# Kernel tuning notes

Measured on AMD Instinct MI355X. Metric: run time of the kernel, lower is better.

Reference implementation:

```python
import jax, jax.numpy as jnp
import numpy as np

N_ROW = 50000
N_COL = 50000
E = 600000
D = 128
NEG_SLOPE = 0.01  # torch LeakyReLU default


def _leaky(x):
    return jnp.where(x >= 0, x, NEG_SLOPE * x)


def _mlp(x, W1, b1, W2, b2):
    # (Linear -> LeakyReLU) x2, matching nn.Sequential in Conv_layer
    h = _leaky(x @ W1 + b1)
    return _leaky(h @ W2 + b2)


def setup_inputs() -> dict:
    key = jax.random.key(0)
    ks = jax.random.split(key, 16)
    inp = {
        "feat_row": jax.random.normal(ks[0], (N_ROW, D), jnp.float32),
        "feat_col": jax.random.normal(ks[1], (N_COL, D), jnp.float32),
        "src_c2r": jax.random.randint(ks[2], (E,), 0, N_COL, jnp.int32),
        "dst_c2r": jax.random.randint(ks[3], (E,), 0, N_ROW, jnp.int32),
        "w_c2r": jax.random.uniform(ks[4], (E,), jnp.float32),
        "src_r2c": jax.random.randint(ks[5], (E,), 0, N_ROW, jnp.int32),
        "dst_r2c": jax.random.randint(ks[6], (E,), 0, N_COL, jnp.int32),
        "w_r2c": jax.random.uniform(ks[7], (E,), jnp.float32),
        "W1_c2r": jax.random.normal(ks[8], (D, D), jnp.float32) / np.sqrt(D),
        "b1_c2r": jax.random.normal(ks[9], (D,), jnp.float32) * 0.01,
        "W2_c2r": jax.random.normal(ks[10], (D, D), jnp.float32) / np.sqrt(D),
        "b2_c2r": jax.random.normal(ks[11], (D,), jnp.float32) * 0.01,
        "W1_r2c": jax.random.normal(ks[12], (D, D), jnp.float32) / np.sqrt(D),
        "b1_r2c": jax.random.normal(ks[13], (D,), jnp.float32) * 0.01,
        "W2_r2c": jax.random.normal(ks[14], (D, D), jnp.float32) / np.sqrt(D),
        "b2_r2c": jax.random.normal(ks[15], (D,), jnp.float32) * 0.01,
        "eps_c2r": jnp.zeros((), jnp.float32),  # DGL GINConv init_eps=0
        "eps_r2c": jnp.zeros((), jnp.float32),
    }
    return inp


def reference(feat_row, feat_col, src_c2r, dst_c2r, w_c2r, src_r2c, dst_r2c, w_r2c,
              W1_c2r, b1_c2r, W2_c2r, b2_c2r, W1_r2c, b1_r2c, W2_r2c, b2_r2c,
              eps_c2r, eps_r2c):
    # col -> row GINConv (edge-weighted sum aggregation)
    msg = feat_col[src_c2r] * w_c2r[:, None]                       # [E, D]
    agg_row = jax.ops.segment_sum(msg, dst_c2r, num_segments=N_ROW)
    h_row = _mlp((1.0 + eps_c2r) * feat_row + agg_row, W1_c2r, b1_c2r, W2_c2r, b2_c2r)
    # row -> col GINConv using updated row features
    msg2 = h_row[src_r2c] * w_r2c[:, None]                         # [E, D]
    agg_col = jax.ops.segment_sum(msg2, dst_r2c, num_segments=N_COL)
    h_col = _mlp((1.0 + eps_r2c) * feat_col + agg_col, W1_r2c, b1_r2c, W2_r2c, b2_r2c)
    # residual (use_residual=True): add pre-conv embeddings
    return h_row + feat_row, h_col + feat_col
```

## Files before the change

kernel.cpp:

```cpp
#include <hip/hip_runtime.h>
#include <hip/hip_bf16.h>

#define NROW 50000
#define NCOL 50000
#define DDIM 128
#define CAP  32

typedef __bf16 bf16_t;
typedef __bf16 bf16x2 __attribute__((ext_vector_type(2)));
typedef __bf16 bf16x8 __attribute__((ext_vector_type(8)));
typedef float  f32x4  __attribute__((ext_vector_type(4)));

__device__ __forceinline__ float lrelu(float v) { return v >= 0.f ? v : 0.01f * v; }

__device__ __forceinline__ float ldf(const void* p, size_t i, bool f) {
    return f ? ((const float*)p)[i] : (float)((const bf16_t*)p)[i];
}

__device__ __forceinline__ bool dtf(const int* flags, int fi) {
    return (fi == -1) ? true : (fi == -2) ? false : (flags[fi] != 0);
}

struct TensorTab { const void* p[18]; int n[18]; };

__global__ __launch_bounds__(256) void detect_dtypes(TensorTab T, int* flags)
{
    __shared__ int vb, vf;
    const int tid = threadIdx.x;
    for (int t = 0; t < 18; ++t) {
        if (tid == 0) { vb = 0; vf = 0; }
        __syncthreads();
        const int n = T.n[t];
        const bool isFloatArr = (t != 2 && t != 3 && t != 5 && t != 6) && n >= 2;
        if (isFloatArr) {
            int nw = n / 2;
            int wi = (int)(((long long)tid * nw) >> 8);
            unsigned w = ((const unsigned*)T.p[t])[wi];
            unsigned low = w & 0xffffu;
            if (low) {
                int e = (int)((low >> 7) & 0xffu);
                if (e >= 90 && e <= 141) atomicAdd(&vb, 1);
                else                     atomicAdd(&vf, 1);
            }
        }
        __syncthreads();
        if (tid == 0) flags[t] = (isFloatArr && vf > vb) ? 1 : 0;
        __syncthreads();
    }
}

struct WPtrs { const void* W[4]; int fi[4]; };

__global__ __launch_bounds__(256) void prep_weights(WPtrs P, const int* flags,
                                                    __bf16* outp)
{
    int slot = blockIdx.x * 256 + threadIdx.x;
    if (slot >= 4 * 2048) return;
    int m = slot >> 11, sIdx = slot & 2047;
    bool f = flags[P.fi[m]] != 0;
    int l = sIdx & 63, combo = sIdx >> 6;
    int ct = combo >> 2, kk = combo & 3;
    int col  = ct * 16 + (l & 15);
    int krow = kk * 32 + (l >> 4) * 8;
    bf16x8 v;
#pragma unroll
    for (int j = 0; j < 8; ++j)
        v[j] = (__bf16)ldf(P.W[m], (size_t)(krow + j) * DDIM + col, f);
    ((bf16x8*)outp)[slot] = v;
}

__global__ __launch_bounds__(256) void convert_bf16(
    const void* __restrict__ in, __bf16* __restrict__ out, int n8,
    const int* __restrict__ flags, int fi)
{
    const bool f = dtf(flags, fi);
    int i = blockIdx.x * 256 + threadIdx.x;
    if (i >= n8) return;
    bf16x8 v;
    if (f) {
        f32x4 a = ((const f32x4*)in)[i * 2];
        f32x4 b = ((const f32x4*)in)[i * 2 + 1];
#pragma unroll
        for (int j = 0; j < 4; ++j) { v[j] = (__bf16)a[j]; v[j + 4] = (__bf16)b[j]; }
    } else {
        v = ((const bf16x8*)in)[i];
    }
    ((bf16x8*)out)[i] = v;
}

__global__ __launch_bounds__(256) void fill_slots_packed(
    const int* __restrict__ dst, const int* __restrict__ srcArr,
    const void* __restrict__ wArr, int nE, int* __restrict__ counts,
    int2* __restrict__ slots2, int* __restrict__ ovCount,
    int* __restrict__ ovList, const int* __restrict__ flags, int fiW)
{
    int e = blockIdx.x * 256 + threadIdx.x;
    if (e >= nE) return;
    const bool fW = dtf(flags, fiW);
    int d = dst[e];
    int pos = atomicAdd(&counts[d], 1);
    if (pos < CAP) {
        int2 pk;
        pk.x = srcArr[e];
        pk.y = __float_as_int(ldf(wArr, e, fW));
        slots2[(size_t)d * CAP + pos] = pk;
    } else {
        int k = atomicAdd(ovCount, 1);
        ovList[k] = e;
    }
}

__global__ __launch_bounds__(256) void scatter_overflow(
    const void* __restrict__ feat, const int* __restrict__ srcArr,
    const int* __restrict__ dstArr, const void* __restrict__ wArr,
    const int* __restrict__ ovList, const int* __restrict__ ovCount,
    float* __restrict__ agg, const int* __restrict__ flags, int fiFeat, int fiW)
{
    const bool fF = dtf(flags, fiFeat);
    const bool fW = dtf(flags, fiW);
    const int nOv = *ovCount;
    const int stride = gridDim.x * 256;
    for (int g = blockIdx.x * 256 + threadIdx.x; (g >> 5) < nOv; g += stride) {
        int idx = g >> 5;
        int e = ovList[idx];
        int c = (g & 31) << 2;
        int s = srcArr[e], d = dstArr[e];
        float wf = ldf(wArr, e, fW);
        size_t base = (size_t)s * DDIM + c;
        float* ap = agg + (size_t)d * DDIM + c;
        unsafeAtomicAdd(ap + 0, ldf(feat, base + 0, fF) * wf);
        unsafeAtomicAdd(ap + 1, ldf(feat, base + 1, fF) * wf);
        unsafeAtomicAdd(ap + 2, ldf(feat, base + 2, fF) * wf);
        unsafeAtomicAdd(ap + 3, ldf(feat, base + 3, fF) * wf);
    }
}

__global__ __launch_bounds__(256) void segsum_b(
    const __bf16* __restrict__ gsrc, const int* __restrict__ counts,
    const int2* __restrict__ slots2, float* __restrict__ agg, int nRows)
{
    int row = blockIdx.x * 4 + (threadIdx.x >> 6);
    if (row >= nRows) return;
    int lane = threadIdx.x & 63;

    int cnt = counts[row]; if (cnt > CAP) cnt = CAP;

    int sr = 0; float wv = 0.f;
    if (lane < cnt) {
        int2 pk = slots2[(size_t)row * CAP + lane];
        sr = pk.x;
        wv = __int_as_float(pk.y);
    }

    float2* ap = (float2*)(agg + (size_t)row * DDIM) + lane;
    float2 acc0 = {0.f, 0.f}, acc1 = {0.f, 0.f};

    const bf16x2* fb = (const bf16x2*)gsrc;
    int i = 0;
    for (; i + 4 <= cnt; i += 4) {
        int   a0 = __shfl(sr, i),     a1 = __shfl(sr, i + 1);
        int   a2 = __shfl(sr, i + 2), a3 = __shfl(sr, i + 3);
        float w0 = __shfl(wv, i),     w1 = __shfl(wv, i + 1);
        float w2 = __shfl(wv, i + 2), w3 = __shfl(wv, i + 3);
        bf16x2 v0 = fb[(size_t)a0 * 64 + lane];
        bf16x2 v1 = fb[(size_t)a1 * 64 + lane];
        bf16x2 v2 = fb[(size_t)a2 * 64 + lane];
        bf16x2 v3 = fb[(size_t)a3 * 64 + lane];
        acc0.x += (float)v0[0] * w0; acc0.y += (float)v0[1] * w0;
        acc1.x += (float)v1[0] * w1; acc1.y += (float)v1[1] * w1;
        acc0.x += (float)v2[0] * w2; acc0.y += (float)v2[1] * w2;
        acc1.x += (float)v3[0] * w3; acc1.y += (float)v3[1] * w3;
    }
    for (; i < cnt; ++i) {
        int   a0 = __shfl(sr, i);
        float w0 = __shfl(wv, i);
        bf16x2 v0 = fb[(size_t)a0 * 64 + lane];
        acc0.x += (float)v0[0] * w0; acc0.y += (float)v0[1] * w0;
    }
    acc0.x += acc1.x; acc0.y += acc1.y;
    *ap = acc0;
}

__global__ __launch_bounds__(256) void fill_slots(
    const int* __restrict__ dst, int nE, int* __restrict__ counts,
    int* __restrict__ slots, int* __restrict__ ovCount, int* __restrict__ ovList,
    const void* __restrict__ feat, const int* __restrict__ srcArr,
    const void* __restrict__ wArr, float* __restrict__ agg,
    const int* __restrict__ flags, int fiFeat, int fiW)
{
    int e = blockIdx.x * 256 + threadIdx.x;
    if (e >= nE) return;
    int d = dst[e];
    int pos = atomicAdd(&counts[d], 1);
    if (pos < CAP) {
        slots[(size_t)d * CAP + pos] = e;
    } else if (ovList) {
        int k = atomicAdd(ovCount, 1);
        ovList[k] = e;
    } else {
        const bool fF = dtf(flags, fiFeat);
        const bool fW = dtf(flags, fiW);
        int s = srcArr[e];
        float wf = ldf(wArr, e, fW);
        for (int c = 0; c < DDIM; ++c)
            unsafeAtomicAdd(&agg[(size_t)d * DDIM + c],
                            ldf(feat, (size_t)s * DDIM + c, fF) * wf);
    }
}

template <bool ZINIT>
__global__ __launch_bounds__(256) void segsum(
    const void* __restrict__ feat, const int* __restrict__ srcArr,
    const void* __restrict__ wArr, const int* __restrict__ counts,
    const int* __restrict__ slots, float* __restrict__ agg, int nRows,
    const int* __restrict__ flags, int fiFeat, int fiW)
{
    const bool fF = dtf(flags, fiFeat);
    const bool fW = dtf(flags, fiW);
    int row = blockIdx.x * 4 + (threadIdx.x >> 6);
    if (row >= nRows) return;
    int lane = threadIdx.x & 63;

    int cnt = counts[row]; if (cnt > CAP) cnt = CAP;

    int sr = 0; float wv = 0.f;
    if (lane < cnt) {
        int e = slots[(size_t)row * CAP + lane];
        sr = srcArr[e];
        wv = ldf(wArr, e, fW);
    }

    float2* ap = (float2*)(agg + (size_t)row * DDIM) + lane;
    float2 acc0 = {0.f, 0.f}, acc1 = {0.f, 0.f};
    if (!ZINIT) acc0 = *ap;

    if (fF) {
        const float2* fb = (const float2*)feat;
        int i = 0;
        for (; i + 4 <= cnt; i += 4) {
            int   a0 = __shfl(sr, i),     a1 = __shfl(sr, i + 1);
            int   a2 = __shfl(sr, i + 2), a3 = __shfl(sr, i + 3);
            float w0 = __shfl(wv, i),     w1 = __shfl(wv, i + 1);
            float w2 = __shfl(wv, i + 2), w3 = __shfl(wv, i + 3);
            float2 v0 = fb[(size_t)a0 * 64 + lane];
            float2 v1 = fb[(size_t)a1 * 64 + lane];
            float2 v2 = fb[(size_t)a2 * 64 + lane];
            float2 v3 = fb[(size_t)a3 * 64 + lane];
            acc0.x += v0.x * w0; acc0.y += v0.y * w0;
            acc1.x += v1.x * w1; acc1.y += v1.y * w1;
            acc0.x += v2.x * w2; acc0.y += v2.y * w2;
            acc1.x += v3.x * w3; acc1.y += v3.y * w3;
        }
        for (; i < cnt; ++i) {
            int   a0 = __shfl(sr, i);
            float w0 = __shfl(wv, i);
            float2 v0 = fb[(size_t)a0 * 64 + lane];
            acc0.x += v0.x * w0; acc0.y += v0.y * w0;
        }
    } else {
        const bf16x2* fb = (const bf16x2*)feat;
        int i = 0;
        for (; i + 4 <= cnt; i += 4) {
            int   a0 = __shfl(sr, i),     a1 = __shfl(sr, i + 1);
            int   a2 = __shfl(sr, i + 2), a3 = __shfl(sr, i + 3);
            float w0 = __shfl(wv, i),     w1 = __shfl(wv, i + 1);
            float w2 = __shfl(wv, i + 2), w3 = __shfl(wv, i + 3);
            bf16x2 v0 = fb[(size_t)a0 * 64 + lane];
            bf16x2 v1 = fb[(size_t)a1 * 64 + lane];
            bf16x2 v2 = fb[(size_t)a2 * 64 + lane];
            bf16x2 v3 = fb[(size_t)a3 * 64 + lane];
            acc0.x += (float)v0[0] * w0; acc0.y += (float)v0[1] * w0;
            acc1.x += (float)v1[0] * w1; acc1.y += (float)v1[1] * w1;
            acc0.x += (float)v2[0] * w2; acc0.y += (float)v2[1] * w2;
            acc1.x += (float)v3[0] * w3; acc1.y += (float)v3[1] * w3;
        }
        for (; i < cnt; ++i) {
            int   a0 = __shfl(sr, i);
            float w0 = __shfl(wv, i);
            bf16x2 v0 = fb[(size_t)a0 * 64 + lane];
            acc0.x += (float)v0[0] * w0; acc0.y += (float)v0[1] * w0;
        }
    }
    acc0.x += acc1.x; acc0.y += acc1.y;
    *ap = acc0;
}

__global__ __launch_bounds__(256) void scatter_any(
    const void* __restrict__ feat, const int* __restrict__ src,
    const int* __restrict__ dst, const void* __restrict__ w,
    float* __restrict__ agg, int nE,
    const int* __restrict__ flags, int fiFeat, int fiW)
{
    const bool fF = dtf(flags, fiFeat);
    const bool fW = dtf(flags, fiW);
    int g = blockIdx.x * 256 + threadIdx.x;
    int e = g >> 5;
    if (e >= nE) return;
    int c = (g & 31) << 2;
    int s = src[e], d = dst[e];
    float wf = ldf(w, e, fW);
    size_t base = (size_t)s * DDIM + c;
    float* ap = agg + (size_t)d * DDIM + c;
    unsafeAtomicAdd(ap + 0, ldf(feat, base + 0, fF) * wf);
    unsafeAtomicAdd(ap + 1, ldf(feat, base + 1, fF) * wf);
    unsafeAtomicAdd(ap + 2, ldf(feat, base + 2, fF) * wf);
    unsafeAtomicAdd(ap + 3, ldf(feat, base + 3, fF) * wf);
}

__global__ __launch_bounds__(256) void residual_add(
    float* __restrict__ out, const void* __restrict__ feat, int n4,
    const int* __restrict__ flags, int fiFeat)
{
    const bool fF = flags[fiFeat] != 0;
    int i = blockIdx.x * 256 + threadIdx.x;
    if (i >= n4) return;
    f32x4 o = ((const f32x4*)out)[i];
    f32x4 r;
#pragma unroll
    for (int j = 0; j < 4; ++j) r[j] = o[j] + ldf(feat, (size_t)i * 4 + j, fF);
    ((f32x4*)out)[i] = r;
}

__device__ __forceinline__ void fill_wfrag(const void* __restrict__ W, bool f,
                                           __bf16* wf, int tid)
{
#pragma unroll
    for (int i = 0; i < 8; ++i) {
        int sIdx  = tid + i * 256;
        int l     = sIdx & 63;
        int combo = sIdx >> 6;
        int ct = combo >> 2, kk = combo & 3;
        int col  = ct * 16 + (l & 15);
        int krow = kk * 32 + (l >> 4) * 8;
        __bf16* dp = wf + (size_t)sIdx * 8;
#pragma unroll
        for (int j = 0; j < 8; ++j)
            dp[j] = (__bf16)ldf(W, (size_t)(krow + j) * DDIM + col, f);
    }
}

__device__ __forceinline__ void copy_wfrag(const __bf16* __restrict__ prep,
                                           __bf16* wf, int tid)
{
    const f32x4* sp = (const f32x4*)prep;
    f32x4* dp = (f32x4*)wf;
#pragma unroll
    for (int i = 0; i < 8; ++i) dp[tid + i * 256] = sp[tid + i * 256];
}

template <bool RESIDUAL, bool PREP>
__global__ __launch_bounds__(256) void mlp_kernel(
    const void* __restrict__ feat, const float* __restrict__ agg,
    const void* __restrict__ W1, const void* __restrict__ b1,
    const void* __restrict__ W2, const void* __restrict__ b2,
    const void* __restrict__ epsp, float* __restrict__ out, int N,
    const int* __restrict__ flags,
    int fiFeat, int fiW1, int fiB1, int fiW2, int fiB2, int fiEps,
    const __bf16* __restrict__ pW1, const __bf16* __restrict__ pW2,
    __bf16* __restrict__ hout)
{
    __shared__ alignas(16) __bf16 wf[32 * 64 * 8];
    __shared__ alignas(16) __bf16 h1t[64 * 136];

    const bool fF  = flags[fiFeat] != 0;
    const bool fB1 = flags[fiB1] != 0;
    const bool fB2 = flags[fiB2] != 0;
    const bool fE  = flags[fiEps] != 0;

    const int tid  = threadIdx.x;
    const int lane = tid & 63;
    const int wave = tid >> 6;
    const int quad = lane >> 4;
    const int r    = lane & 15;

    if (PREP) copy_wfrag(pW1, wf, tid);
    else      fill_wfrag(W1, flags[fiW1] != 0, wf, tid);

    const float eps1 = 1.f + ldf(epsp, 0, fE);
    const int rowBase = blockIdx.x * 64 + wave * 16;

    bf16x8 a[4];
    {
        int rowA = rowBase + r;
        if (rowA < N) {
            size_t fb = (size_t)rowA * DDIM + quad * 8;
            const f32x4* gp = (const f32x4*)(agg + fb);
            if (fF) {
                const f32x4* fp = (const f32x4*)((const float*)feat + fb);
#pragma unroll
                for (int kk = 0; kk < 4; ++kk) {
                    f32x4 f0 = fp[kk * 8], f1 = fp[kk * 8 + 1];
                    f32x4 g0 = gp[kk * 8], g1 = gp[kk * 8 + 1];
                    bf16x8 av;
#pragma unroll
                    for (int j = 0; j < 4; ++j) {
                        av[j]     = (__bf16)(f0[j] * eps1 + g0[j]);
                        av[j + 4] = (__bf16)(f1[j] * eps1 + g1[j]);
                    }
                    a[kk] = av;
                }
            } else {
                const bf16x8* fp = (const bf16x8*)((const bf16_t*)feat + fb);
#pragma unroll
                for (int kk = 0; kk < 4; ++kk) {
                    bf16x8 fv = fp[kk * 4];
                    f32x4 g0 = gp[kk * 8], g1 = gp[kk * 8 + 1];
                    bf16x8 av;
#pragma unroll
                    for (int j = 0; j < 4; ++j) {
                        av[j]     = (__bf16)((float)fv[j]     * eps1 + g0[j]);
                        av[j + 4] = (__bf16)((float)fv[j + 4] * eps1 + g1[j]);
                    }
                    a[kk] = av;
                }
            }
        } else {
#pragma unroll
            for (int kk = 0; kk < 4; ++kk)
#pragma unroll
                for (int j = 0; j < 8; ++j) a[kk][j] = (__bf16)0.f;
        }
    }

    __syncthreads();

    const bf16x8* wv = (const bf16x8*)wf;
#pragma unroll
    for (int ct = 0; ct < 8; ++ct) {
        f32x4 acc = {0.f, 0.f, 0.f, 0.f};
#pragma unroll
        for (int kk = 0; kk < 4; ++kk)
            acc = __builtin_amdgcn_mfma_f32_16x16x32_bf16(
                a[kk], wv[(ct * 4 + kk) * 64 + lane], acc, 0, 0, 0);
        float bias = ldf(b1, ct * 16 + r, fB1);
#pragma unroll
        for (int gg = 0; gg < 4; ++gg)
            h1t[(wave * 16 + quad * 4 + gg) * 136 + ct * 16 + r] =
                (__bf16)lrelu(acc[gg] + bias);
    }
    __syncthreads();

    bf16x8 a2[4];
#pragma unroll
    for (int kk = 0; kk < 4; ++kk)
        a2[kk] = *(const bf16x8*)&h1t[(wave * 16 + r) * 136 + kk * 32 + quad * 8];

    if (PREP) copy_wfrag(pW2, wf, tid);
    else      fill_wfrag(W2, flags[fiW2] != 0, wf, tid);
    __syncthreads();

#pragma unroll
    for (int ct = 0; ct < 8; ++ct) {
        f32x4 acc = {0.f, 0.f, 0.f, 0.f};
#pragma unroll
        for (int kk = 0; kk < 4; ++kk)
            acc = __builtin_amdgcn_mfma_f32_16x16x32_bf16(
                a2[kk], wv[(ct * 4 + kk) * 64 + lane], acc, 0, 0, 0);
        float bias = ldf(b2, ct * 16 + r, fB2);
#pragma unroll
        for (int gg = 0; gg < 4; ++gg) {
            int row = rowBase + quad * 4 + gg;
            if (row < N) {
                int col = ct * 16 + r;
                float v = lrelu(acc[gg] + bias);
                if (hout) hout[(size_t)row * DDIM + col] = (__bf16)v;
                if (RESIDUAL) v += ldf(feat, (size_t)row * DDIM + col, fF);
                out[(size_t)row * DDIM + col] = v;
            }
        }
    }
}

extern "C" void kernel_launch(void* const* d_in, const int* in_sizes, int n_in,
                              void* d_out, int out_size, void* d_ws, size_t ws_size,
                              hipStream_t stream)
{
    const int* src_c2r = (const int*)d_in[2];
    const int* dst_c2r = (const int*)d_in[3];
    const int* src_r2c = (const int*)d_in[5];
    const int* dst_r2c = (const int*)d_in[6];
    const int nE = in_sizes[2];

    char* wsb = (char*)d_ws;
    int*    flags  = (int*)wsb;
    __bf16* wfprep = (__bf16*)(wsb + 128);
    int*    counts = (int*)(wsb + 128 + 131072);
    int*    ovCnt  = counts + NROW;
    size_t  ofs    = 128 + 131072 + ((size_t)NROW + 8) * 4;
    ofs = (ofs + 15) & ~(size_t)15;
    int2*   slots2 = (int2*)(wsb + ofs);
    int*    slots  = (int*)(wsb + ofs);
    size_t  ofsOvA = ofs + (size_t)NROW * CAP * 8;
    size_t  ofsOvB = ofs + (size_t)NROW * CAP * 4;
    int*    ovListA = (int*)(wsb + ofsOvA);
    int*    ovListB = (int*)(wsb + ofsOvB);
    size_t  ofsCb  = (ofsOvA + (size_t)nE * 4 + 15) & ~(size_t)15;
    __bf16* cbuf   = (__bf16*)(wsb + ofsCb);

    const size_t NEED_A = ofsCb + (size_t)NROW * DDIM * 2;
    const size_t NEED_B = ofsOvB + (size_t)nE * 4;
    const size_t NEED_B0 = ofsOvB;
    const bool tierA  = ws_size >= NEED_A;
    const bool tierB  = ws_size >= NEED_B;
    const bool tierB0 = ws_size >= NEED_B0;

    TensorTab T;
    for (int i = 0; i < 18; ++i) { T.p[i] = d_in[i]; T.n[i] = in_sizes[i]; }

    float* out_row = (float*)d_out;
    float* out_col = out_row + (size_t)NROW * DDIM;
    const size_t aggBytes = (size_t)NROW * DDIM * sizeof(float);

    const int eblocks  = (nE + 255) / 256;
    const int sblocks  = (nE * 32 + 255) / 256;
    const int mblocksR = (NROW + 63) / 64;
    const int mblocksC = (NCOL + 63) / 64;
    const int gblocksR = (NROW + 3) / 4;
    const int gblocksC = (NCOL + 3) / 4;
    const int cblocks  = (NROW * DDIM / 8 + 255) / 256;

    detect_dtypes<<<1, 256, 0, stream>>>(T, flags);

    if (tierA) {
        WPtrs P;
        P.W[0] = d_in[8];  P.fi[0] = 8;
        P.W[1] = d_in[10]; P.fi[1] = 10;
        P.W[2] = d_in[12]; P.fi[2] = 12;
        P.W[3] = d_in[14]; P.fi[3] = 14;
        prep_weights<<<32, 256, 0, stream>>>(P, flags, wfprep);

        convert_bf16<<<cblocks, 256, 0, stream>>>(d_in[1], cbuf,
            NCOL * DDIM / 8, flags, 1);
        hipMemsetAsync(counts, 0, ((size_t)NROW + 8) * 4, stream);
        fill_slots_packed<<<eblocks, 256, 0, stream>>>(dst_c2r, src_c2r,
            d_in[4], nE, counts, slots2, ovCnt, ovListA, flags, 4);
        segsum_b<<<gblocksR, 256, 0, stream>>>(cbuf, counts, slots2,
            out_col, NROW);
        scatter_overflow<<<256, 256, 0, stream>>>(d_in[1], src_c2r,
            dst_c2r, d_in[4], ovListA, ovCnt, out_col, flags, 1, 4);
        mlp_kernel<true, true><<<mblocksR, 256, 0, stream>>>(
            d_in[0], out_col, d_in[8], d_in[9], d_in[10], d_in[11], d_in[16],
            out_row, NROW, flags, 0, 8, 9, 10, 11, 16,
            wfprep + 0 * 16384, wfprep + 1 * 16384, cbuf);

        hipMemsetAsync(counts, 0, ((size_t)NROW + 8) * 4, stream);
        fill_slots_packed<<<eblocks, 256, 0, stream>>>(dst_r2c, src_r2c,
            d_in[7], nE, counts, slots2, ovCnt, ovListA, flags, 7);
        segsum_b<<<gblocksC, 256, 0, stream>>>(cbuf, counts, slots2,
            out_col, NCOL);
        scatter_overflow<<<256, 256, 0, stream>>>(cbuf, src_r2c,
            dst_r2c, d_in[7], ovListA, ovCnt, out_col, flags, -2, 7);
        mlp_kernel<true, true><<<mblocksC, 256, 0, stream>>>(
            d_in[1], out_col, d_in[12], d_in[13], d_in[14], d_in[15], d_in[17],
            out_col, NCOL, flags, 1, 12, 13, 14, 15, 17,
            wfprep + 2 * 16384, wfprep + 3 * 16384, nullptr);
    } else if (tierB0) {
        WPtrs P;
        P.W[0] = d_in[8];  P.fi[0] = 8;
        P.W[1] = d_in[10]; P.fi[1] = 10;
        P.W[2] = d_in[12]; P.fi[2] = 12;
        P.W[3] = d_in[14]; P.fi[3] = 14;
        prep_weights<<<32, 256, 0, stream>>>(P, flags, wfprep);

        hipMemsetAsync(counts, 0, ((size_t)NROW + 8) * 4, stream);
        if (!tierB) hipMemsetAsync(out_col, 0, aggBytes, stream);
        fill_slots<<<eblocks, 256, 0, stream>>>(dst_c2r, nE, counts, slots,
            ovCnt, tierB ? ovListB : nullptr,
            d_in[1], src_c2r, d_in[4], out_col, flags, 1, 4);
        if (tierB) {
            segsum<true><<<gblocksR, 256, 0, stream>>>(d_in[1], src_c2r,
                d_in[4], counts, slots, out_col, NROW, flags, 1, 4);
            scatter_overflow<<<256, 256, 0, stream>>>(d_in[1], src_c2r,
                dst_c2r, d_in[4], ovListB, ovCnt, out_col, flags, 1, 4);
        } else {
            segsum<false><<<gblocksR, 256, 0, stream>>>(d_in[1], src_c2r,
                d_in[4], counts, slots, out_col, NROW, flags, 1, 4);
        }
        mlp_kernel<false, true><<<mblocksR, 256, 0, stream>>>(
            d_in[0], out_col, d_in[8], d_in[9], d_in[10], d_in[11], d_in[16],
            out_row, NROW, flags, 0, 8, 9, 10, 11, 16,
            wfprep + 0 * 16384, wfprep + 1 * 16384, nullptr);

        hipMemsetAsync(counts, 0, ((size_t)NROW + 8) * 4, stream);
        if (!tierB) hipMemsetAsync(out_col, 0, aggBytes, stream);
        fill_slots<<<eblocks, 256, 0, stream>>>(dst_r2c, nE, counts, slots,
            ovCnt, tierB ? ovListB : nullptr,
            out_row, src_r2c, d_in[7], out_col, flags, -1, 7);
        if (tierB) {
            segsum<true><<<gblocksC, 256, 0, stream>>>(out_row, src_r2c,
                d_in[7], counts, slots, out_col, NCOL, flags, -1, 7);
            scatter_overflow<<<256, 256, 0, stream>>>(out_row, src_r2c,
                dst_r2c, d_in[7], ovListB, ovCnt, out_col, flags, -1, 7);
        } else {
            segsum<false><<<gblocksC, 256, 0, stream>>>(out_row, src_r2c,
                d_in[7], counts, slots, out_col, NCOL, flags, -1, 7);
        }
        residual_add<<<(NROW * DDIM / 4 + 255) / 256, 256, 0, stream>>>(
            out_row, d_in[0], NROW * DDIM / 4, flags, 0);
        mlp_kernel<true, true><<<mblocksC, 256, 0, stream>>>(
            d_in[1], out_col, d_in[12], d_in[13], d_in[14], d_in[15], d_in[17],
            out_col, NCOL, flags, 1, 12, 13, 14, 15, 17,
            wfprep + 2 * 16384, wfprep + 3 * 16384, nullptr);
    } else {
        hipMemsetAsync(out_col, 0, aggBytes, stream);
        scatter_any<<<sblocks, 256, 0, stream>>>(d_in[1], src_c2r, dst_c2r,
            d_in[4], out_col, nE, flags, 1, 4);
        mlp_kernel<false, false><<<mblocksR, 256, 0, stream>>>(
            d_in[0], out_col, d_in[8], d_in[9], d_in[10], d_in[11], d_in[16],
            out_row, NROW, flags, 0, 8, 9, 10, 11, 16, nullptr, nullptr, nullptr);

        hipMemsetAsync(out_col, 0, aggBytes, stream);
        scatter_any<<<sblocks, 256, 0, stream>>>(out_row, src_r2c, dst_r2c,
            d_in[7], out_col, nE, flags, -1, 7);
        residual_add<<<(NROW * DDIM / 4 + 255) / 256, 256, 0, stream>>>(
            out_row, d_in[0], NROW * DDIM / 4, flags, 0);
        mlp_kernel<true, false><<<mblocksC, 256, 0, stream>>>(
            d_in[1], out_col, d_in[12], d_in[13], d_in[14], d_in[15], d_in[17],
            out_col, NCOL, flags, 1, 12, 13, 14, 15, 17, nullptr, nullptr, nullptr);
    }
}
```

Baseline: 371.0 us.

## Fuse prep, overflow scatter and count zeroing into fewer kernels; register-resident MLP weights

Merges weight prep, feature bf16 conversion and counts zeroing into one launch. Overflow edges are now handled by extra blocks inside the segment-sum kernel, which zero overflowing rows up front and accumulate atomically, replacing a separate scatter kernel. A new MLP kernel holds pre-swizzled weights in registers instead of staging them in LDS, writes the bf16 hidden output through LDS with coalesced stores, and zeroes counts for the next pass. Dtype detection is parallelized across 18 blocks. The aim is fewer launches and less serialization, at the cost of high register pressure and a dependence on atomic ordering for overflowed rows.

```diff
diff --git a/kernel.cpp b/kernel.cpp
--- a/kernel.cpp
+++ b/kernel.cpp
@@ -27,72 +27,75 @@
 {
     __shared__ int vb, vf;
     const int tid = threadIdx.x;
-    for (int t = 0; t < 18; ++t) {
-        if (tid == 0) { vb = 0; vf = 0; }
-        __syncthreads();
-        const int n = T.n[t];
-        const bool isFloatArr = (t != 2 && t != 3 && t != 5 && t != 6) && n >= 2;
-        if (isFloatArr) {
-            int nw = n / 2;
-            int wi = (int)(((long long)tid * nw) >> 8);
-            unsigned w = ((const unsigned*)T.p[t])[wi];
-            unsigned low = w & 0xffffu;
-            if (low) {
-                int e = (int)((low >> 7) & 0xffu);
-                if (e >= 90 && e <= 141) atomicAdd(&vb, 1);
-                else                     atomicAdd(&vf, 1);
-            }
-        }
-        __syncthreads();
-        if (tid == 0) flags[t] = (isFloatArr && vf > vb) ? 1 : 0;
-        __syncthreads();
-    }
+    const int t = blockIdx.x;
+    if (tid == 0) { vb = 0; vf = 0; }
+    __syncthreads();
+    const int n = T.n[t];
+    const bool isFloatArr = (t != 2 && t != 3 && t != 5 && t != 6) && n >= 2;
+    if (isFloatArr) {
+        int nw = n / 2;
+        int wi = (int)(((long long)tid * nw) >> 8);
+        unsigned w = ((const unsigned*)T.p[t])[wi];
+        unsigned low = w & 0xffffu;
+        if (low) {
+            int e = (int)((low >> 7) & 0xffu);
+            if (e >= 90 && e <= 141) atomicAdd(&vb, 1);
+            else                     atomicAdd(&vf, 1);
+        }
+    }
+    __syncthreads();
+    if (tid == 0) flags[t] = (isFloatArr && vf > vb) ? 1 : 0;
 }
 
 struct WPtrs { const void* W[4]; int fi[4]; };
 
-__global__ __launch_bounds__(256) void prep_weights(WPtrs P, const int* flags,
-                                                    __bf16* outp)
-{
-    int slot = blockIdx.x * 256 + threadIdx.x;
-    if (slot >= 4 * 2048) return;
-    int m = slot >> 11, sIdx = slot & 2047;
-    bool f = flags[P.fi[m]] != 0;
-    int l = sIdx & 63, combo = sIdx >> 6;
-    int ct = combo >> 2, kk = combo & 3;
-    int col  = ct * 16 + (l & 15);
-    int krow = kk * 32 + (l >> 4) * 8;
-    bf16x8 v;
-#pragma unroll
-    for (int j = 0; j < 8; ++j)
-        v[j] = (__bf16)ldf(P.W[m], (size_t)(krow + j) * DDIM + col, f);
-    ((bf16x8*)outp)[slot] = v;
-}
-
-__global__ __launch_bounds__(256) void convert_bf16(
-    const void* __restrict__ in, __bf16* __restrict__ out, int n8,
-    const int* __restrict__ flags, int fi)
-{
-    const bool f = dtf(flags, fi);
-    int i = blockIdx.x * 256 + threadIdx.x;
-    if (i >= n8) return;
-    bf16x8 v;
-    if (f) {
-        f32x4 a = ((const f32x4*)in)[i * 2];
-        f32x4 b = ((const f32x4*)in)[i * 2 + 1];
-#pragma unroll
-        for (int j = 0; j < 4; ++j) { v[j] = (__bf16)a[j]; v[j + 4] = (__bf16)b[j]; }
+__global__ __launch_bounds__(256) void prep_all(
+    WPtrs P, const int* __restrict__ flags, __bf16* __restrict__ wfp,
+    const void* __restrict__ feat, __bf16* __restrict__ cbuf, int n8, int fiFeat,
+    int* __restrict__ zc, int zn, int cblocks, int zblocks)
+{
+    const int b = blockIdx.x;
+    const int tid = threadIdx.x;
+    if (b < cblocks) {
+        int i = b * 256 + tid;
+        if (i >= n8) return;
+        const bool f = dtf(flags, fiFeat);
+        bf16x8 v;
+        if (f) {
+            f32x4 a = ((const f32x4*)feat)[i * 2];
+            f32x4 c = ((const f32x4*)feat)[i * 2 + 1];
+#pragma unroll
+            for (int j = 0; j < 4; ++j) { v[j] = (__bf16)a[j]; v[j + 4] = (__bf16)c[j]; }
+        } else {
+            v = ((const bf16x8*)feat)[i];
+        }
+        ((bf16x8*)cbuf)[i] = v;
+    } else if (b < cblocks + zblocks) {
+        int i = (b - cblocks) * 256 + tid;
+        if (i < zn) zc[i] = 0;
     } else {
-        v = ((const bf16x8*)in)[i];
-    }
-    ((bf16x8*)out)[i] = v;
+        int slot = (b - cblocks - zblocks) * 256 + tid;
+        if (slot >= 4 * 2048) return;
+        int m = slot >> 11, sIdx = slot & 2047;
+        bool f = flags[P.fi[m]] != 0;
+        int l = sIdx & 63, combo = sIdx >> 6;
+        int ct = combo >> 2, kk = combo & 3;
+        int col  = ct * 16 + (l & 15);
+        int krow = kk * 32 + (l >> 4) * 8;
+        bf16x8 v;
+#pragma unroll
+        for (int j = 0; j < 8; ++j)
+            v[j] = (__bf16)ldf(P.W[m], (size_t)(krow + j) * DDIM + col, f);
+        ((bf16x8*)wfp)[slot] = v;
+    }
 }
 
 __global__ __launch_bounds__(256) void fill_slots_packed(
     const int* __restrict__ dst, const int* __restrict__ srcArr,
     const void* __restrict__ wArr, int nE, int* __restrict__ counts,
     int2* __restrict__ slots2, int* __restrict__ ovCount,
-    int* __restrict__ ovList, const int* __restrict__ flags, int fiW)
+    int* __restrict__ ovList, float* __restrict__ agg,
+    const int* __restrict__ flags, int fiW)
 {
     int e = blockIdx.x * 256 + threadIdx.x;
     if (e >= nE) return;
@@ -105,45 +108,50 @@
         pk.y = __float_as_int(ldf(wArr, e, fW));
         slots2[(size_t)d * CAP + pos] = pk;
     } else {
+        if (pos == CAP) {
+            f32x4 z = {0.f, 0.f, 0.f, 0.f};
+            f32x4* rp = (f32x4*)(agg + (size_t)d * DDIM);
+#pragma unroll 4
+            for (int c = 0; c < DDIM / 4; ++c) rp[c] = z;
+        }
         int k = atomicAdd(ovCount, 1);
         ovList[k] = e;
     }
 }
 
-__global__ __launch_bounds__(256) void scatter_overflow(
-    const void* __restrict__ feat, const int* __restrict__ srcArr,
-    const int* __restrict__ dstArr, const void* __restrict__ wArr,
-    const int* __restrict__ ovList, const int* __restrict__ ovCount,
-    float* __restrict__ agg, const int* __restrict__ flags, int fiFeat, int fiW)
-{
-    const bool fF = dtf(flags, fiFeat);
-    const bool fW = dtf(flags, fiW);
-    const int nOv = *ovCount;
-    const int stride = gridDim.x * 256;
-    for (int g = blockIdx.x * 256 + threadIdx.x; (g >> 5) < nOv; g += stride) {
-        int idx = g >> 5;
-        int e = ovList[idx];
-        int c = (g & 31) << 2;
-        int s = srcArr[e], d = dstArr[e];
-        float wf = ldf(wArr, e, fW);
-        size_t base = (size_t)s * DDIM + c;
-        float* ap = agg + (size_t)d * DDIM + c;
-        unsafeAtomicAdd(ap + 0, ldf(feat, base + 0, fF) * wf);
-        unsafeAtomicAdd(ap + 1, ldf(feat, base + 1, fF) * wf);
-        unsafeAtomicAdd(ap + 2, ldf(feat, base + 2, fF) * wf);
-        unsafeAtomicAdd(ap + 3, ldf(feat, base + 3, fF) * wf);
-    }
-}
-
-__global__ __launch_bounds__(256) void segsum_b(
+__global__ __launch_bounds__(256) void segsum_ov(
     const __bf16* __restrict__ gsrc, const int* __restrict__ counts,
-    const int2* __restrict__ slots2, float* __restrict__ agg, int nRows)
-{
-    int row = blockIdx.x * 4 + (threadIdx.x >> 6);
+    const int2* __restrict__ slots2, float* __restrict__ agg, int nRows,
+    const int* __restrict__ srcArr, const int* __restrict__ dstArr,
+    const void* __restrict__ wArr, const int* __restrict__ ovList,
+    const int* __restrict__ ovCount, const int* __restrict__ flags, int fiW,
+    int gblocks)
+{
+    const int tid  = threadIdx.x;
+    const int lane = tid & 63;
+
+    if ((int)blockIdx.x >= gblocks) {
+        const bool fW = dtf(flags, fiW);
+        const int nOv = *ovCount;
+        const int wv_ = tid >> 6;
+        const int nWaves = 64 * 4;
+        for (int k = (blockIdx.x - gblocks) * 4 + wv_; k < nOv; k += nWaves) {
+            int e = ovList[k];
+            int s = srcArr[e], d = dstArr[e];
+            float wf = ldf(wArr, e, fW);
+            bf16x2 v = ((const bf16x2*)gsrc)[(size_t)s * 64 + lane];
+            float* ap = agg + (size_t)d * DDIM + lane * 2;
+            unsafeAtomicAdd(ap + 0, (float)v[0] * wf);
+            unsafeAtomicAdd(ap + 1, (float)v[1] * wf);
+        }
+        return;
+    }
+
+    int row = blockIdx.x * 4 + (tid >> 6);
     if (row >= nRows) return;
-    int lane = threadIdx.x & 63;
-
-    int cnt = counts[row]; if (cnt > CAP) cnt = CAP;
+
+    int cntRaw = counts[row];
+    int cnt = cntRaw > CAP ? CAP : cntRaw;
 
     int sr = 0; float wv = 0.f;
     if (lane < cnt) {
@@ -178,7 +186,156 @@
         acc0.x += (float)v0[0] * w0; acc0.y += (float)v0[1] * w0;
     }
     acc0.x += acc1.x; acc0.y += acc1.y;
-    *ap = acc0;
+    if (cntRaw > CAP) {
+        unsafeAtomicAdd(&ap->x, acc0.x);
+        unsafeAtomicAdd(&ap->y, acc0.y);
+    } else {
+        *ap = acc0;
+    }
+}
+
+template <bool RESIDUAL, bool HOUT>
+__global__ __launch_bounds__(256) void mlp_reg(
+    const void* __restrict__ feat, const float* __restrict__ agg,
+    const void* __restrict__ b1, const void* __restrict__ b2,
+    const void* __restrict__ epsp, float* __restrict__ out, int N,
+    const int* __restrict__ flags, int fiFeat, int fiB1, int fiB2, int fiEps,
+    const __bf16* __restrict__ pW1, const __bf16* __restrict__ pW2,
+    __bf16* __restrict__ hout, int* __restrict__ zc, int zn)
+{
+    __shared__ alignas(16) __bf16 h1t[64 * 136];
+
+    const int tid  = threadIdx.x;
+    if (zc) {
+        int gi = blockIdx.x * 256 + tid;
+        if (gi < zn) zc[gi] = 0;
+    }
+
+    const bool fF  = flags[fiFeat] != 0;
+    const bool fB1 = flags[fiB1] != 0;
+    const bool fB2 = flags[fiB2] != 0;
+    const bool fE  = flags[fiEps] != 0;
+
+    const int lane = tid & 63;
+    const int wave = tid >> 6;
+    const int quad = lane >> 4;
+    const int r    = lane & 15;
+    const int rowBase = blockIdx.x * 64 + wave * 16;
+
+    const bf16x8* pw1v = (const bf16x8*)pW1;
+    bf16x8 w1f[32];
+#pragma unroll
+    for (int i = 0; i < 32; ++i) w1f[i] = pw1v[i * 64 + lane];
+
+    float bias1[8];
+#pragma unroll
+    for (int ct = 0; ct < 8; ++ct) bias1[ct] = ldf(b1, ct * 16 + r, fB1);
+    const float eps1 = 1.f + ldf(epsp, 0, fE);
+
+    bf16x8 a[4];
+    {
+        int rowA = rowBase + r;
+        if (rowA < N) {
+            size_t fb = (size_t)rowA * DDIM + quad * 8;
+            const f32x4* gp = (const f32x4*)(agg + fb);
+            if (fF) {
+                const f32x4* fp = (const f32x4*)((const float*)feat + fb);
+#pragma unroll
+                for (int kk = 0; kk < 4; ++kk) {
+                    f32x4 f0 = fp[kk * 8], f1 = fp[kk * 8 + 1];
+                    f32x4 g0 = gp[kk * 8], g1 = gp[kk * 8 + 1];
+                    bf16x8 av;
+#pragma unroll
+                    for (int j = 0; j < 4; ++j) {
+                        av[j]     = (__bf16)(f0[j] * eps1 + g0[j]);
+                        av[j + 4] = (__bf16)(f1[j] * eps1 + g1[j]);
+                    }
+                    a[kk] = av;
+                }
+            } else {
+                const bf16x8* fp = (const bf16x8*)((const bf16_t*)feat + fb);
+#pragma unroll
+                for (int kk = 0; kk < 4; ++kk) {
+                    bf16x8 fv = fp[kk * 4];
+                    f32x4 g0 = gp[kk * 8], g1 = gp[kk * 8 + 1];
+                    bf16x8 av;
+#pragma unroll
+                    for (int j = 0; j < 4; ++j) {
+                        av[j]     = (__bf16)((float)fv[j]     * eps1 + g0[j]);
+                        av[j + 4] = (__bf16)((float)fv[j + 4] * eps1 + g1[j]);
+                    }
+                    a[kk] = av;
+                }
+            }
+        } else {
+#pragma unroll
+            for (int kk = 0; kk < 4; ++kk)
+#pragma unroll
+                for (int j = 0; j < 8; ++j) a[kk][j] = (__bf16)0.f;
+        }
+    }
+
+#pragma unroll
+    for (int ct = 0; ct < 8; ++ct) {
+        f32x4 acc = {0.f, 0.f, 0.f, 0.f};
+#pragma unroll
+        for (int kk = 0; kk < 4; ++kk)
+            acc = __builtin_amdgcn_mfma_f32_16x16x32_bf16(
+                a[kk], w1f[ct * 4 + kk], acc, 0, 0, 0);
+#pragma unroll
+        for (int gg = 0; gg < 4; ++gg)
+            h1t[(wave * 16 + quad * 4 + gg) * 136 + ct * 16 + r] =
+                (__bf16)lrelu(acc[gg] + bias1[ct]);
+    }
+
+    bf16x8 a2[4];
+#pragma unroll
+    for (int kk = 0; kk < 4; ++kk)
+        a2[kk] = *(const bf16x8*)&h1t[(wave * 16 + r) * 136 + kk * 32 + quad * 8];
+
+    const bf16x8* pw2v = (const bf16x8*)pW2;
+    bf16x8 w2f[32];
+#pragma unroll
+    for (int i = 0; i < 32; ++i) w2f[i] = pw2v[i * 64 + lane];
+    float bias2[8];
+#pragma unroll
+    for (int ct = 0; ct < 8; ++ct) bias2[ct] = ldf(b2, ct * 16 + r, fB2);
+
+#pragma unroll
+    for (int ct = 0; ct < 8; ++ct) {
+        f32x4 acc = {0.f, 0.f, 0.f, 0.f};
+#pragma unroll
+        for (int kk = 0; kk < 4; ++kk)
+            acc = __builtin_amdgcn_mfma_f32_16x16x32_bf16(
+                a2[kk], w2f[ct * 4 + kk], acc, 0, 0, 0);
+#pragma unroll
+        for (int gg = 0; gg < 4; ++gg) {
+            int row = rowBase + quad * 4 + gg;
+            float v = lrelu(acc[gg] + bias2[ct]);
+            if (HOUT)
+                h1t[(wave * 16 + quad * 4 + gg) * 136 + ct * 16 + r] = (__bf16)v;
+            if (row < N) {
+                int col = ct * 16 + r;
+                if (RESIDUAL) v += ldf(feat, (size_t)row * DDIM + col, fF);
+                out[(size_t)row * DDIM + col] = v;
+            }
+        }
+    }
+
+    if (HOUT) {
+        __syncthreads();
+        const int blockBase = blockIdx.x * 64;
+#pragma unroll
+        for (int c = 0; c < 4; ++c) {
+            int chunk = tid + c * 256;
+            int row = chunk >> 4;
+            int k   = (chunk & 15) * 8;
+            if (blockBase + row < N) {
+                bf16x8 v = *(const bf16x8*)&h1t[row * 136 + k];
+                *(bf16x8*)&hout[(size_t)(blockBase + row) * DDIM + k] = v;
+            }
+        }
+    }
 }
 
 __global__ __launch_bounds__(256) void fill_slots(
@@ -208,6 +365,31 @@
     }
 }
 
+__global__ __launch_bounds__(256) void scatter_overflow(
+    const void* __restrict__ feat, const int* __restrict__ srcArr,
+    const int* __restrict__ dstArr, const void* __restrict__ wArr,
+    const int* __restrict__ ovList, const int* __restrict__ ovCount,
+    float* __restrict__ agg, const int* __restrict__ flags, int fiFeat, int fiW)
+{
+    const bool fF = dtf(flags, fiFeat);
+    const bool fW = dtf(flags, fiW);
+    const int nOv = *ovCount;
+    const int stride = gridDim.x * 256;
+    for (int g = blockIdx.x * 256 + threadIdx.x; (g >> 5) < nOv; g += stride) {
+        int idx = g >> 5;
+        int e = ovList[idx];
+        int c = (g & 31) << 2;
+        int s = srcArr[e], d = dstArr[e];
+        float wf = ldf(wArr, e, fW);
+        size_t base = (size_t)s * DDIM + c;
+        float* ap = agg + (size_t)d * DDIM + c;
+        unsafeAtomicAdd(ap + 0, ldf(feat, base + 0, fF) * wf);
+        unsafeAtomicAdd(ap + 1, ldf(feat, base + 1, fF) * wf);
+        unsafeAtomicAdd(ap + 2, ldf(feat, base + 2, fF) * wf);
+        unsafeAtomicAdd(ap + 3, ldf(feat, base + 3, fF) * wf);
+    }
+}
+
 template <bool ZINIT>
 __global__ __launch_bounds__(256) void segsum(
     const void* __restrict__ feat, const int* __restrict__ srcArr,
@@ -356,8 +538,7 @@
     const void* __restrict__ epsp, float* __restrict__ out, int N,
     const int* __restrict__ flags,
     int fiFeat, int fiW1, int fiB1, int fiW2, int fiB2, int fiEps,
-    const __bf16* __restrict__ pW1, const __bf16* __restrict__ pW2,
-    __bf16* __restrict__ hout)
+    const __bf16* __restrict__ pW1, const __bf16* __restrict__ pW2)
 {
     __shared__ alignas(16) __bf16 wf[32 * 64 * 8];
     __shared__ alignas(16) __bf16 h1t[64 * 136];
@@ -463,7 +644,6 @@
             if (row < N) {
                 int col = ct * 16 + r;
                 float v = lrelu(acc[gg] + bias);
-                if (hout) hout[(size_t)row * DDIM + col] = (__bf16)v;
                 if (RESIDUAL) v += ldf(feat, (size_t)row * DDIM + col, fF);
                 out[(size_t)row * DDIM + col] = v;
             }
@@ -497,8 +677,8 @@
     size_t  ofsCb  = (ofsOvA + (size_t)nE * 4 + 15) & ~(size_t)15;
     __bf16* cbuf   = (__bf16*)(wsb + ofsCb);
 
-    const size_t NEED_A = ofsCb + (size_t)NROW * DDIM * 2;
-    const size_t NEED_B = ofsOvB + (size_t)nE * 4;
+    const size_t NEED_A  = ofsCb + (size_t)NROW * DDIM * 2;
+    const size_t NEED_B  = ofsOvB + (size_t)nE * 4;
     const size_t NEED_B0 = ofsOvB;
     const bool tierA  = ws_size >= NEED_A;
     const bool tierB  = ws_size >= NEED_B;
@@ -517,9 +697,11 @@
     const int mblocksC = (NCOL + 63) / 64;
     const int gblocksR = (NROW + 3) / 4;
     const int gblocksC = (NCOL + 3) / 4;
-    const int cblocks  = (NROW * DDIM / 8 + 255) / 256;
-
-    detect_dtypes<<<1, 256, 0, stream>>>(T, flags);
+    const int cblocks  = (NCOL * DDIM / 8 + 255) / 256;
+    const int zblocks  = ((NROW + 8) + 255) / 256;
+    const int zn       = NROW + 8;
+
+    detect_dtypes<<<18, 256, 0, stream>>>(T, flags);
 
     if (tierA) {
         WPtrs P;
@@ -527,40 +709,38 @@
         P.W[1] = d_in[10]; P.fi[1] = 10;
         P.W[2] = d_in[12]; P.fi[2] = 12;
         P.W[3] = d_in[14]; P.fi[3] = 14;
-        prep_weights<<<32, 256, 0, stream>>>(P, flags, wfprep);
-
-        convert_bf16<<<cblocks, 256, 0, stream>>>(d_in[1], cbuf,
-            NCOL * DDIM / 8, flags, 1);
-        hipMemsetAsync(counts, 0, ((size_t)NROW + 8) * 4, stream);
+
+        prep_all<<<cblocks + zblocks + 32, 256, 0, stream>>>(
+            P, flags, wfprep, d_in[1], cbuf, NCOL * DDIM / 8, 1,
+            counts, zn, cblocks, zblocks);
+
         fill_slots_packed<<<eblocks, 256, 0, stream>>>(dst_c2r, src_c2r,
-            d_in[4], nE, counts, slots2, ovCnt, ovListA, flags, 4);
-        segsum_b<<<gblocksR, 256, 0, stream>>>(cbuf, counts, slots2,
-            out_col, NROW);
-        scatter_overflow<<<256, 256, 0, stream>>>(d_in[1], src_c2r,
-            dst_c2r, d_in[4], ovListA, ovCnt, out_col, flags, 1, 4);
-        mlp_kernel<true, true><<<mblocksR, 256, 0, stream>>>(
-            d_in[0], out_col, d_in[8], d_in[9], d_in[10], d_in[11], d_in[16],
-            out_row, NROW, flags, 0, 8, 9, 10, 11, 16,
-            wfprep + 0 * 16384, wfprep + 1 * 16384, cbuf);
-
-        hipMemsetAsync(counts, 0, ((size_t)NROW + 8) * 4, stream);
+            d_in[4], nE, counts, slots2, ovCnt, ovListA, out_col, flags, 4);
+        segsum_ov<<<gblocksR + 64, 256, 0, stream>>>(cbuf, counts, slots2,
+            out_col, NROW, src_c2r, dst_c2r, d_in[4], ovListA, ovCnt,
+            flags, 4, gblocksR);
+        mlp_reg<true, true><<<mblocksR, 256, 0, stream>>>(
+            d_in[0], out_col, d_in[9], d_in[11], d_in[16],
+            out_row, NROW, flags, 0, 9, 11, 16,
+            wfprep + 0 * 16384, wfprep + 1 * 16384, cbuf, counts, zn);
+
         fill_slots_packed<<<eblocks, 256, 0, stream>>>(dst_r2c, src_r2c,
-            d_in[7], nE, counts, slots2, ovCnt, ovListA, flags, 7);
-        segsum_b<<<gblocksC, 256, 0, stream>>>(cbuf, counts, slots2,
-            out_col, NCOL);
-        scatter_overflow<<<256, 256, 0, stream>>>(cbuf, src_r2c,
-            dst_r2c, d_in[7], ovListA, ovCnt, out_col, flags, -2, 7);
-        mlp_kernel<true, true><<<mblocksC, 256, 0, stream>>>(
-            d_in[1], out_col, d_in[12], d_in[13], d_in[14], d_in[15], d_in[17],
-            out_col, NCOL, flags, 1, 12, 13, 14, 15, 17,
-            wfprep + 2 * 16384, wfprep + 3 * 16384, nullptr);
+            d_in[7], nE, counts, slots2, ovCnt, ovListA, out_col, flags, 7);
+        segsum_ov<<<gblocksC + 64, 256, 0, stream>>>(cbuf, counts, slots2,
+            out_col, NCOL, src_r2c, dst_r2c, d_in[7], ovListA, ovCnt,
+            flags, 7, gblocksC);
+        mlp_reg<true, false><<<mblocksC, 256, 0, stream>>>(
+            d_in[1], out_col, d_in[13], d_in[15], d_in[17],
+            out_col, NCOL, flags, 1, 13, 15, 17,
+            wfprep + 2 * 16384, wfprep + 3 * 16384, nullptr, nullptr, 0);
     } else if (tierB0) {
         WPtrs P;
         P.W[0] = d_in[8];  P.fi[0] = 8;
         P.W[1] = d_in[10]; P.fi[1] = 10;
         P.W[2] = d_in[12]; P.fi[2] = 12;
         P.W[3] = d_in[14]; P.fi[3] = 14;
-        prep_weights<<<32, 256, 0, stream>>>(P, flags, wfprep);
+        prep_all<<<32, 256, 0, stream>>>(P, flags, wfprep,
+            nullptr, nullptr, 0, -1, nullptr, 0, 0, 0);
 
         hipMemsetAsync(counts, 0, ((size_t)NROW + 8) * 4, stream);
         if (!tierB) hipMemsetAsync(out_col, 0, aggBytes, stream);
@@ -579,7 +759,7 @@
         mlp_kernel<false, true><<<mblocksR, 256, 0, stream>>>(
             d_in[0], out_col, d_in[8], d_in[9], d_in[10], d_in[11], d_in[16],
             out_row, NROW, flags, 0, 8, 9, 10, 11, 16,
-            wfprep + 0 * 16384, wfprep + 1 * 16384, nullptr);
+            wfprep + 0 * 16384, wfprep + 1 * 16384);
 
         hipMemsetAsync(counts, 0, ((size_t)NROW + 8) * 4, stream);
         if (!tierB) hipMemsetAsync(out_col, 0, aggBytes, stream);
@@ -600,14 +780,14 @@
         mlp_kernel<true, true><<<mblocksC, 256, 0, stream>>>(
             d_in[1], out_col, d_in[12], d_in[13], d_in[14], d_in[15], d_in[17],
             out_col, NCOL, flags, 1, 12, 13, 14, 15, 17,
-            wfprep + 2 * 16384, wfprep + 3 * 16384, nullptr);
+            wfprep + 2 * 16384, wfprep + 3 * 16384);
     } else {
         hipMemsetAsync(out_col, 0, aggBytes, stream);
         scatter_any<<<sblocks, 256, 0, stream>>>(d_in[1], src_c2r, dst_c2r,
             d_in[4], out_col, nE, flags, 1, 4);
         mlp_kernel<false, false><<<mblocksR, 256, 0, stream>>>(
             d_in[0], out_col, d_in[8], d_in[9], d_in[10], d_in[11], d_in[16],
-            out_row, NROW, flags, 0, 8, 9, 10, 11, 16, nullptr, nullptr, nullptr);
+            out_row, NROW, flags, 0, 8, 9, 10, 11, 16, nullptr, nullptr);
 
         hipMemsetAsync(out_col, 0, aggBytes, stream);
         scatter_any<<<sblocks, 256, 0, stream>>>(out_row, src_r2c, dst_r2c,
@@ -616,6 +796,6 @@
             out_row, d_in[0], NROW * DDIM / 4, flags, 0);
         mlp_kernel<true, false><<<mblocksC, 256, 0, stream>>>(
             d_in[1], out_col, d_in[12], d_in[13], d_in[14], d_in[15], d_in[17],
-            out_col, NCOL, flags, 1, 12, 13, 14, 15, 17, nullptr, nullptr, nullptr);
-    }
-}
+            out_col, NCOL, flags, 1, 12, 13, 14, 15, 17, nullptr, nullptr);
+    }
+}
```

After: 340.0 us. 1.09x faster.
